# Performance work log

Measured on AMD Instinct MI355X. Metric: run time of the kernel, lower is better.

The kernel has to match this reference:

```python
import jax, jax.numpy as jnp
import numpy as np
import math

N_NODES = 50000
N_EDGES = 800000
IN_DIM = 128
HID = 128
OUT_DIM = 2048
N_LABEL_EDGES = 4096
POOL_RATIO = 0.5
NUM_HEADS = 8


def seg_sum(x, idx, n):
    return jax.ops.segment_sum(x, idx, num_segments=n)


def graph_conv(x, W, b, src, dst, emask, n):
    # DGL GraphConv, norm='both': D_out^-1/2 A D_in^-1/2 (x W) + b (masked edges)
    deg_out = seg_sum(emask, src, n)
    deg_in = seg_sum(emask, dst, n)
    ns = jax.lax.rsqrt(jnp.maximum(deg_out, 1.0))
    nd = jax.lax.rsqrt(jnp.maximum(deg_in, 1.0))
    h = x @ W
    msg = (h * ns[:, None])[src] * emask[:, None]
    agg = seg_sum(msg, dst, n)
    return agg * nd[:, None] + b


def conv_pool_block(x, src, dst, emask, cW, cb, sW, sb):
    # GraphConv -> ReLU -> SAGPool(top-k by GraphConv score, tanh gate) -> avg||max readout
    n = x.shape[0]
    h = jax.nn.relu(graph_conv(x, cW, cb, src, dst, emask, n))
    score = graph_conv(h, sW, sb, src, dst, emask, n)[:, 0]
    k = int(math.ceil(POOL_RATIO * n))  # static
    _, perm = jax.lax.top_k(score, k)
    h_new = h[perm] * jnp.tanh(score[perm])[:, None]
    # remap edges to the pooled node set; drop edges touching removed nodes via mask
    newid = jnp.full((n,), -1, jnp.int32).at[perm].set(jnp.arange(k, dtype=jnp.int32))
    nsrc = newid[src]
    ndst = newid[dst]
    new_mask = emask * (nsrc >= 0).astype(emask.dtype) * (ndst >= 0).astype(emask.dtype)
    nsrc = jnp.maximum(nsrc, 0)
    ndst = jnp.maximum(ndst, 0)
    readout = jnp.concatenate([h_new.mean(0), h_new.max(0)])[None, :]  # [1, 2*HID]
    return h_new, nsrc, ndst, new_mask, readout


def gat_conv(x, fcW, al, ar, lsrc, ldst, n, slope=0.2):
    # GATConv(1 -> 1, num_heads=8): head feature dim is 1
    h = x @ fcW                      # [n, heads]
    el = h * al
    er = h * ar
    e = jax.nn.leaky_relu(el[lsrc] + er[ldst], slope)  # [E_l, heads]
    emax = jax.ops.segment_max(e, ldst, num_segments=n)
    emax = jnp.where(jnp.isfinite(emax), emax, 0.0)
    ex = jnp.exp(e - emax[ldst])
    denom = seg_sum(ex, ldst, n)
    alpha = ex / jnp.maximum(denom[ldst], 1e-9)
    out = seg_sum(alpha * h[lsrc], ldst, n)            # [n, heads]
    return out[:, :, None]                             # [n, heads, 1]


def setup_inputs() -> dict:
    key = jax.random.key(0)
    ks = jax.random.split(key, 32)

    def rn(k, shape, s=0.05):
        return jax.random.normal(k, shape, jnp.float32) * s

    inp = {}
    inp['feat'] = jax.random.normal(ks[0], (N_NODES, IN_DIM), jnp.float32)
    inp['sequence_feature'] = jax.random.normal(ks[1], (1, 1024), jnp.float32)
    inp['src'] = jax.random.randint(ks[2], (N_EDGES,), 0, N_NODES, jnp.int32)
    inp['dst'] = jax.random.randint(ks[3], (N_EDGES,), 0, N_NODES, jnp.int32)
    inp['label_src'] = jax.random.randint(ks[4], (N_LABEL_EDGES,), 0, OUT_DIM, jnp.int32)
    inp['label_dst'] = jax.random.randint(ks[5], (N_LABEL_EDGES,), 0, OUT_DIM, jnp.int32)
    i = 6
    for b in range(3):
        din = IN_DIM if b == 0 else HID
        inp['cW%d' % b] = rn(ks[i], (din, HID)); i += 1
        inp['cb%d' % b] = jnp.zeros((HID,), jnp.float32)
        inp['sW%d' % b] = rn(ks[i], (HID, 1)); i += 1
        inp['sb%d' % b] = jnp.zeros((1,), jnp.float32)
    inp['lin1W'] = rn(ks[i], (2 * HID + 1024, 2 * HID)); i += 1
    inp['lin1b'] = jnp.zeros((2 * HID,), jnp.float32)
    inp['lin2W'] = rn(ks[i], (2 * HID, HID)); i += 1
    inp['lin2b'] = jnp.zeros((HID,), jnp.float32)
    inp['lin3W'] = rn(ks[i], (HID, OUT_DIM)); i += 1
    inp['lin3b'] = jnp.zeros((OUT_DIM,), jnp.float32)
    inp['gat_fcW'] = rn(ks[i], (1, NUM_HEADS)); i += 1
    inp['gat_al'] = rn(ks[i], (NUM_HEADS,)); i += 1
    inp['gat_ar'] = rn(ks[i], (NUM_HEADS,)); i += 1
    return inp


def reference(feat, sequence_feature, src, dst, label_src, label_dst,
              cW0, cb0, sW0, sb0, cW1, cb1, sW1, sb1, cW2, cb2, sW2, sb2,
              lin1W, lin1b, lin2W, lin2b, lin3W, lin3b,
              gat_fcW, gat_al, gat_ar):
    x, s, d = feat, src, dst
    emask = jnp.ones((src.shape[0],), jnp.float32)
    final = None
    for cW, cb, sW, sb in ((cW0, cb0, sW0, sb0), (cW1, cb1, sW1, sb1), (cW2, cb2, sW2, sb2)):
        x, s, d, emask, ro = conv_pool_block(x, s, d, emask, cW, cb, sW, sb)
        final = ro if final is None else final + ro
    final = jnp.concatenate([final, sequence_feature], axis=-1)  # [1, 2*HID+1024]
    f = jax.nn.relu(final @ lin1W + lin1b)
    # dropout: eval mode -> identity
    f = jax.nn.relu(f @ lin2W + lin2b)
    f = f @ lin3W + lin3b          # [1, OUT_DIM]
    ft = f.T                       # [OUT_DIM, 1]
    gat_out = gat_conv(ft, gat_fcW, gat_al, gat_ar, label_src, label_dst, OUT_DIM)
    max_value = jnp.max(gat_out, axis=1)      # [OUT_DIM, 1]
    _ = ft - jax.nn.relu(max_value)           # computed then discarded, as in source
    return ft.T
```

## Files before the change

kernel.cpp:

```cpp
#include <hip/hip_runtime.h>
#include <hip/hip_bf16.h>
#include <cmath>

#define N0 50000
#define NEDGE 800000
#define NEG_HUGE -3.402823466e38f
#define BMAX 64
#define STRIDE 128

typedef int i32x4 __attribute__((ext_vector_type(4)));
typedef __attribute__((ext_vector_type(8))) short short8v;
typedef __attribute__((ext_vector_type(4))) float f32x4;

__device__ inline float b2f(unsigned short u) { return __uint_as_float(((unsigned)u) << 16); }

__device__ inline unsigned short f2b(float f) {
    __hip_bfloat16 h = __float2bfloat16(f);
    return *(unsigned short*)&h;
}

__device__ inline unsigned fkey(float f) {
    unsigned b = __float_as_uint(f);
    if (b == 0x80000000u) b = 0u;
    return (b & 0x80000000u) ? ~b : (b | 0x80000000u);
}

__device__ inline void atomicMaxF(float* a, float v) {
    if (v >= 0.f) atomicMax((int*)a, __float_as_int(v));
    else          atomicMin((unsigned int*)a, __float_as_uint(v));
}

__global__ void k_init(float* finalv, float* f1raw, int* deg_out, int* fill,
                       int* binsA, int* binsB, float* maxbuf, int* ctrl) {
    int i = blockIdx.x * blockDim.x + threadIdx.x;
    if (i < 256) { finalv[i] = 0.f; f1raw[i] = 0.f; }
    if (i < 384) maxbuf[i] = NEG_HUGE;
    if (i < N0) { deg_out[i] = 0; fill[i] = 0; }
    if (i < 65536) { binsA[i] = 0; binsB[i] = 0; }
    if (i < 2) ctrl[8 + i] = 0;
}

__global__ __launch_bounds__(256) void k_remap(
        const int* __restrict__ esrc, const int* __restrict__ edst,
        const int2* __restrict__ ein, int use_pair,
        const int* __restrict__ ctrl, int slot,
        const int* __restrict__ newid,
        int2* __restrict__ eout, int* __restrict__ outcnt) {
    __shared__ int wbase[4];
    __shared__ int blkbase;
    int E = (slot < 0) ? NEDGE : ctrl[slot];
    if (blockIdx.x * 256 >= E) return;
    int i = blockIdx.x * 256 + threadIdx.x;
    int lane = threadIdx.x & 63, w = threadIdx.x >> 6;
    int ns = -1, nd = -1;
    if (i < E) {
        int s, d;
        if (use_pair) { int2 pr = ein[i]; s = pr.x; d = pr.y; }
        else { s = esrc[i]; d = edst[i]; }
        ns = newid[s]; nd = newid[d];
    }
    bool keep = (ns >= 0) && (nd >= 0);
    unsigned long long m = __ballot(keep);
    int rank = __popcll(m & ((1ull << lane) - 1ull));
    if (lane == 0) wbase[w] = __popcll(m);
    __syncthreads();
    if (threadIdx.x == 0)
        blkbase = atomicAdd(outcnt, wbase[0] + wbase[1] + wbase[2] + wbase[3]);
    __syncthreads();
    int base = blkbase;
    for (int q = 0; q < w; ++q) base += wbase[q];
    if (keep) eout[base + rank] = make_int2(ns, nd);
}

__global__ __launch_bounds__(256) void k_build(
        const int* __restrict__ esrc, const int* __restrict__ edst,
        const int2* __restrict__ epair, int use_pair,
        const int* __restrict__ ctrl, int slot, int n, int rsize,
        int* deg_out, int* fill, int* csr_src) {
    int E = (slot < 0) ? NEDGE : ctrl[slot];
    int r = blockIdx.x & 7;
    int lo = r * rsize;
    int hi = min(n, lo + rsize);
    int tpg = (int)(gridDim.x >> 3) * 256;
    int t = (int)(blockIdx.x >> 3) * 256 + threadIdx.x;
    for (int e0 = t * 8; e0 < E; e0 += tpg * 8) {
        int s[8], d[8];
        if (use_pair) {
            const i32x4* pp = (const i32x4*)(epair + e0);
#pragma unroll
            for (int q = 0; q < 4; ++q) {
                i32x4 a = __builtin_nontemporal_load(pp + q);
                s[q * 2] = a.x; d[q * 2] = a.y;
                s[q * 2 + 1] = a.z; d[q * 2 + 1] = a.w;
            }
        } else {
            const i32x4* ps = (const i32x4*)(esrc + e0);
            const i32x4* pd = (const i32x4*)(edst + e0);
#pragma unroll
            for (int q = 0; q < 2; ++q) {
                i32x4 a = __builtin_nontemporal_load(ps + q);
                i32x4 bq = __builtin_nontemporal_load(pd + q);
                s[q * 4] = a.x; s[q * 4 + 1] = a.y; s[q * 4 + 2] = a.z; s[q * 4 + 3] = a.w;
                d[q * 4] = bq.x; d[q * 4 + 1] = bq.y; d[q * 4 + 2] = bq.z; d[q * 4 + 3] = bq.w;
            }
        }
        int nrem = E - e0;
#pragma unroll
        for (int kq = 0; kq < 8; ++kq) {
            if (kq < nrem && d[kq] >= lo && d[kq] < hi) {
                atomicAdd(&deg_out[s[kq]], 1);
                int pos = atomicAdd(&fill[d[kq]], 1);
                if (pos < STRIDE) csr_src[(size_t)d[kq] * STRIDE + pos] = s[kq];
            }
        }
    }
}

__global__ __launch_bounds__(256) void k_gemm(
        const float* __restrict__ feat, const float* __restrict__ xprev,
        const int* __restrict__ oldid, const float* __restrict__ garr,
        const int* __restrict__ deg_out,
        const float* __restrict__ W, unsigned short* __restrict__ hpre,
        int n, int nprev, int mode) {
    __shared__ short Wt[128][136];
    __shared__ int ridx_s[64];
    __shared__ float esc_s[64];
    int tid = threadIdx.x;
    int r0 = blockIdx.x * 64;
    if (tid < 64) {
        int gr = r0 + tid;
        int ridx = 0; float esc = 0.f;
        if (gr < n) {
            if (mode == 0) {
                ridx = gr;
                esc = rsqrtf(fmaxf((float)deg_out[gr], 1.f));
            } else {
                int orow = oldid[gr];
                if ((unsigned)orow < (unsigned)nprev) {
                    ridx = orow;
                    esc = rsqrtf(fmaxf((float)deg_out[gr], 1.f)) * garr[gr];
                }
            }
        }
        ridx_s[tid] = ridx;
        esc_s[tid] = esc;
    }
    {
        int col = tid & 127;
        int kh = tid >> 7;
#pragma unroll
        for (int c8 = 0; c8 < 8; ++c8) {
            int kb = kh * 64 + c8 * 8;
            unsigned short v[8];
#pragma unroll
            for (int j = 0; j < 8; ++j)
                v[j] = f2b(W[(size_t)(kb + j) * 128 + col]);
            *(uint4*)&Wt[col][kb] = *(uint4*)v;
        }
    }
    __syncthreads();

    int lane = tid & 63, w = tid >> 6;
    const float* xsrc = (mode == 0) ? feat : xprev;
    int row16 = lane & 15;
    int ridx = ridx_s[w * 16 + row16];
    int ko = (lane >> 4) * 8;
    f32x4 acc[8];
#pragma unroll
    for (int t = 0; t < 8; ++t) acc[t] = (f32x4){0.f, 0.f, 0.f, 0.f};
#pragma unroll
    for (int kc = 0; kc < 4; ++kc) {
        int kbase = kc * 32 + ko;
        const float4* xp = (const float4*)(xsrc + (size_t)ridx * 128 + kbase);
        float4 fa = xp[0], fb = xp[1];
        unsigned short av[8];
        av[0] = f2b(fa.x); av[1] = f2b(fa.y); av[2] = f2b(fa.z); av[3] = f2b(fa.w);
        av[4] = f2b(fb.x); av[5] = f2b(fb.y); av[6] = f2b(fb.z); av[7] = f2b(fb.w);
        short8v a = *(short8v*)av;
#pragma unroll
        for (int t = 0; t < 8; ++t) {
            short8v b = *(short8v*)&Wt[t * 16 + row16][kbase];
            acc[t] = __builtin_amdgcn_mfma_f32_16x16x32_bf16(a, b, acc[t], 0, 0, 0);
        }
    }
    int rq = (lane >> 4) * 4;
    float esc[4];
#pragma unroll
    for (int r = 0; r < 4; ++r) esc[r] = esc_s[w * 16 + rq + r];
#pragma unroll
    for (int r = 0; r < 4; ++r) {
        int gr = r0 + w * 16 + rq + r;
        if (gr < n) {
            unsigned short* op = hpre + (size_t)gr * 128;
#pragma unroll
            for (int t = 0; t < 8; ++t)
                op[t * 16 + (lane & 15)] = f2b(acc[t][r] * esc[r]);
        }
    }
}

__global__ __launch_bounds__(256) void k_agg_conv(
        const unsigned short* __restrict__ hpre, const int* __restrict__ fill,
        const int* __restrict__ deg_out,
        const int* __restrict__ csr_src,
        const float* __restrict__ cb, const float* __restrict__ sW,
        float* __restrict__ hpost, float* __restrict__ hs, int n) {
    int wid = threadIdx.x >> 6;
    int lane = threadIdx.x & 63;
    int d = blockIdx.x * 4 + wid;
    if (d >= n) return;
    int degin = fill[d];
    int cnt = min(degin, STRIDE);
    const int* bp = csr_src + (size_t)d * STRIDE;
    float a0 = 0.f, a1 = 0.f;
    int j = 0;
    for (; j + 4 <= cnt; j += 4) {
        int4 ss = *(const int4*)(bp + j);
        ushort2 u0 = ((const ushort2*)(hpre + (size_t)ss.x * 128))[lane];
        ushort2 u1 = ((const ushort2*)(hpre + (size_t)ss.y * 128))[lane];
        ushort2 u2 = ((const ushort2*)(hpre + (size_t)ss.z * 128))[lane];
        ushort2 u3 = ((const ushort2*)(hpre + (size_t)ss.w * 128))[lane];
        a0 += (b2f(u0.x) + b2f(u1.x)) + (b2f(u2.x) + b2f(u3.x));
        a1 += (b2f(u0.y) + b2f(u1.y)) + (b2f(u2.y) + b2f(u3.y));
    }
    for (; j < cnt; ++j) {
        int s0 = bp[j];
        ushort2 u0 = ((const ushort2*)(hpre + (size_t)s0 * 128))[lane];
        a0 += b2f(u0.x);
        a1 += b2f(u0.y);
    }
    float nd2 = rsqrtf(fmaxf((float)degin, 1.f));
    int c0 = lane * 2;
    float h0 = fmaxf(fmaf(a0, nd2, cb[c0]), 0.f);
    float h1 = fmaxf(fmaf(a1, nd2, cb[c0 + 1]), 0.f);
    ((float2*)(hpost + (size_t)d * 128))[lane] = make_float2(h0, h1);
    float v = h0 * sW[c0] + h1 * sW[c0 + 1];
#pragma unroll
    for (int off = 32; off; off >>= 1) v += __shfl_down(v, off);
    if (lane == 0) hs[d] = v * rsqrtf(fmaxf((float)deg_out[d], 1.f));
}

__global__ void k_score_hist(const float* __restrict__ hs, const int* __restrict__ fill,
                             const int* __restrict__ csr_src,
                             const float* __restrict__ sb, float* score,
                             int* binsA, int n) {
    int d = blockIdx.x * blockDim.x + threadIdx.x;
    if (d >= n) return;
    int degin = fill[d];
    int cnt = min(degin, STRIDE);
    const int* bp = csr_src + (size_t)d * STRIDE;
    float sum = 0.f;
    int j = 0;
    for (; j + 4 <= cnt; j += 4) {
        int4 ss = *(const int4*)(bp + j);
        sum += (hs[ss.x] + hs[ss.y]) + (hs[ss.z] + hs[ss.w]);
    }
    for (; j < cnt; ++j) sum += hs[bp[j]];
    float sc = rsqrtf(fmaxf((float)degin, 1.f)) * sum + sb[0];
    score[d] = sc;
    atomicAdd(&binsA[fkey(sc) >> 16], 1);
}

__global__ void k_rhist2(const float* __restrict__ score, const int* __restrict__ ctrl,
                         int n, int* binsB) {
    unsigned p16 = (unsigned)ctrl[3];
    for (int i = blockIdx.x * 256 + threadIdx.x; i < n; i += gridDim.x * 256) {
        unsigned u = fkey(score[i]);
        if ((u >> 16) == p16) atomicAdd(&binsB[u & 0xFFFFu], 1);
    }
}

__global__ void k_rpick(int stage, int k0, int* ctrl, const int* __restrict__ bins) {
    __shared__ int gs[64];
    __shared__ int arr[1024];
    __shared__ int wsum[16];
    __shared__ int sChunk, sKrem;
    int t = threadIdx.x;
    {
        int c = t >> 4, sub = t & 15;
        const int4* p4 = (const int4*)(bins + (size_t)c * 1024);
        int s = 0;
#pragma unroll
        for (int q = 0; q < 16; ++q) {
            int4 v = p4[q * 16 + sub];
            s += v.x + v.y + v.z + v.w;
        }
#pragma unroll
        for (int off = 8; off; off >>= 1) s += __shfl_down(s, off, 16);
        if (sub == 0) gs[c] = s;
    }
    __syncthreads();
    if (t == 0) {
        int kneed = (stage == 0) ? k0 : ctrl[4];
        int cum = 0, c = 63;
        for (; c >= 1; --c) { int v = gs[c]; if (cum + v >= kneed) break; cum += v; }
        sChunk = c; sKrem = kneed - cum;
    }
    __syncthreads();
    int c = sChunk;
    int v = bins[(size_t)c * 1024 + t];
    arr[t] = v;
    int lane = t & 63, w = t >> 6;
    int s = v;
#pragma unroll
    for (int off = 32; off; off >>= 1) s += __shfl_down(s, off);
    if (lane == 0) wsum[w] = s;
    __syncthreads();
    if (t == 0) {
        int kneed = sKrem;
        int cum = 0, w2 = 15;
        for (; w2 >= 1; --w2) { int vv = wsum[w2]; if (cum + vv >= kneed) break; cum += vv; }
        int j = 63;
        for (; j >= 1; --j) { int vv = arr[w2 * 64 + j]; if (cum + vv >= kneed) break; cum += vv; }
        int bin = c * 1024 + w2 * 64 + j;
        if (stage == 0) { ctrl[3] = bin; ctrl[4] = kneed - cum; }
        else {
            ctrl[0] = (int)((((unsigned)ctrl[3]) << 16) | (unsigned)bin);
            ctrl[2] = kneed - cum;
        }
    }
}

__global__ void k_ccnt(const float* __restrict__ score, const int* __restrict__ ctrl,
                       int n, int* cntG, int* cntE) {
    __shared__ int wG[16], wE[16];
    int b = blockIdx.x;
    int i = b * 1024 + threadIdx.x;
    int lane = threadIdx.x & 63, wid = threadIdx.x >> 6;
    unsigned T = (unsigned)ctrl[0];
    bool inb = (i < n);
    unsigned u = inb ? fkey(score[i]) : 0u;
    bool isG = inb && (u > T);
    bool isE = inb && (u == T);
    unsigned long long mG = __ballot(isG);
    unsigned long long mE = __ballot(isE);
    if (lane == 0) { wG[wid] = __popcll(mG); wE[wid] = __popcll(mE); }
    __syncthreads();
    if (threadIdx.x == 0) {
        int sg = 0, se = 0;
#pragma unroll
        for (int w = 0; w < 16; ++w) { sg += wG[w]; se += wE[w]; }
        cntG[b] = sg; cntE[b] = se;
    }
}

__global__ void k_cemit(const float* __restrict__ score, const int* __restrict__ ctrl,
                        const int* __restrict__ cntG, const int* __restrict__ cntE,
                        int n, int knext, int* newid, int* oldid, float* garr,
                        int* deg_out, int* fill, int* binsA, int* binsB) {
    __shared__ int wG[16], wE[16];
    __shared__ int sGoff, sEoff;
    int b = blockIdx.x;
    int i = b * 1024 + threadIdx.x;
    if (knext > 0) {
        for (int z = i; z < 65536; z += gridDim.x * 1024) { binsA[z] = 0; binsB[z] = 0; }
        if (i < knext) { deg_out[i] = 0; fill[i] = 0; }
    }
    int lane = threadIdx.x & 63, wid = threadIdx.x >> 6;
    unsigned T = (unsigned)ctrl[0];
    int needEq = ctrl[2];
    bool inb = (i < n);
    float sc = inb ? score[i] : 0.f;
    unsigned u = inb ? fkey(sc) : 0u;
    bool isG = inb && (u > T);
    bool isE = inb && (u == T);
    unsigned long long mG = __ballot(isG);
    unsigned long long mE = __ballot(isE);
    if (lane == 0) { wG[wid] = __popcll(mG); wE[wid] = __popcll(mE); }
    if (threadIdx.x < 64) {
        int l = threadIdx.x;
        int vg = (l < b) ? cntG[l] : 0;
        int ve = (l < b) ? cntE[l] : 0;
#pragma unroll
        for (int off2 = 32; off2; off2 >>= 1) {
            vg += __shfl_down(vg, off2);
            ve += __shfl_down(ve, off2);
        }
        if (l == 0) { sGoff = vg; sEoff = ve; }
    }
    __syncthreads();
    unsigned long long below = (1ull << lane) - 1ull;
    int gW = 0, eW = 0;
    for (int w = 0; w < wid; ++w) { gW += wG[w]; eW += wE[w]; }
    int Gb = sGoff + gW + __popcll(mG & below);
    int Eb = sEoff + eW + __popcll(mE & below);
    if (inb) {
        bool sel = isG || (isE && (Eb < needEq));
        if (sel) {
            int j = Gb + min(Eb, needEq);
            newid[i] = j;
            oldid[j] = i;
            garr[j] = tanhf(sc);
        } else {
            newid[i] = -1;
        }
    }
}

__global__ void k_readout(const float* __restrict__ hpost, const int* __restrict__ oldid,
                          const float* __restrict__ garr, float* finalv, float* maxbuf,
                          int k, int n, float invk) {
    int c = threadIdx.x;
    float sum = 0.f, mx = NEG_HUGE;
    for (int r = blockIdx.x; r < k; r += gridDim.x) {
        int o = oldid[r];
        if ((unsigned)o >= (unsigned)n) continue;
        float g = garr[r];
        float v = hpost[(size_t)o * 128 + c] * g;
        sum += v;
        mx = fmaxf(mx, v);
    }
    atomicAdd(&finalv[c], sum * invk);
    atomicMaxF(&maxbuf[c], mx);
}

__global__ void k_mlp1(const float* __restrict__ finalv, const float* __restrict__ maxbuf,
                       const float* __restrict__ seq, const float* __restrict__ W1,
                       float* f1raw) {
    int o = threadIdx.x;
    int j0 = blockIdx.x * 128;
    float acc = 0.f;
    for (int jj = 0; jj < 128; ++jj) {
        int j = j0 + jj;
        float fv;
        if (j < 128) fv = finalv[j];
        else if (j < 256) fv = maxbuf[j - 128] + maxbuf[j] + maxbuf[j + 128];
        else fv = seq[j - 256];
        acc = fmaf(fv, W1[(size_t)j * 256 + o], acc);
    }
    atomicAdd(&f1raw[o], acc);
}

__global__ void k_mlp2(const float* __restrict__ f1raw, const float* __restrict__ b1,
                       const float* __restrict__ W2, const float* __restrict__ bb2,
                       float* f2v) {
    __shared__ float f1s[256];
    int t = threadIdx.x;
    f1s[t] = fmaxf(f1raw[t] + b1[t], 0.f);
    f1s[t + 128] = fmaxf(f1raw[t + 128] + b1[t + 128], 0.f);
    __syncthreads();
    float acc = 0.f;
    for (int j = 0; j < 256; ++j)
        acc = fmaf(f1s[j], W2[(size_t)j * 128 + t], acc);
    f2v[t] = fmaxf(acc + bb2[t], 0.f);
}

__global__ void k_mlp3(const float* __restrict__ f2v, const float* __restrict__ W3,
                       const float* __restrict__ b3, float* out) {
    __shared__ float f2s[128];
    int t = threadIdx.x;
    f2s[t] = f2v[t];
    __syncthreads();
    int col = blockIdx.x * 128 + t;
    float acc = 0.f;
    for (int j = 0; j < 128; ++j)
        acc = fmaf(f2s[j], W3[(size_t)j * 2048 + col], acc);
    out[col] = acc + b3[col];
}

extern "C" void kernel_launch(void* const* d_in, const int* in_sizes, int n_in,
                              void* d_out, int out_size, void* d_ws, size_t ws_size,
                              hipStream_t stream) {
    (void)in_sizes; (void)n_in; (void)out_size; (void)ws_size;
    const float* feat = (const float*)d_in[0];
    const float* seq  = (const float*)d_in[1];
    const int* src = (const int*)d_in[2];
    const int* dst = (const int*)d_in[3];
    const float *cW[3], *cb[3], *sW[3], *sb[3];
    for (int b = 0; b < 3; ++b) {
        cW[b] = (const float*)d_in[6 + 4 * b];
        cb[b] = (const float*)d_in[7 + 4 * b];
        sW[b] = (const float*)d_in[8 + 4 * b];
        sb[b] = (const float*)d_in[9 + 4 * b];
    }
    const float* lin1W = (const float*)d_in[18];
    const float* lin1b = (const float*)d_in[19];
    const float* lin2W = (const float*)d_in[20];
    const float* lin2b = (const float*)d_in[21];
    const float* lin3W = (const float*)d_in[22];
    const float* lin3b = (const float*)d_in[23];
    float* out = (float*)d_out;

    char* p = (char*)d_ws;
    size_t off = 0;
    auto alloc = [&](size_t bytes) -> void* {
        void* r = p + off;
        off = (off + bytes + 255) & ~(size_t)255;
        return r;
    };
    unsigned short* hpre = (unsigned short*)alloc((size_t)N0 * 128 * 2);
    float* hpost  = (float*)alloc((size_t)N0 * 128 * 4);
    float* hs     = (float*)alloc((size_t)N0 * 4);
    float* score  = (float*)alloc((size_t)N0 * 4);
    int* deg_out  = (int*)alloc((size_t)N0 * 4);
    int* fill     = (int*)alloc((size_t)N0 * 4);
    int2* epair1  = (int2*)alloc((size_t)NEDGE * 8);
    int* csr_src  = (int*)alloc((size_t)N0 * STRIDE * 4);
    int* newid    = (int*)alloc((size_t)N0 * 4);
    int* oldid    = (int*)alloc((size_t)25000 * 4);
    float* garr   = (float*)alloc((size_t)25000 * 4);
    float* maxbuf = (float*)alloc(3 * 128 * 4);
    float* finalv = (float*)alloc(256 * 4);
    float* f1raw  = (float*)alloc(256 * 4);
    float* f2v    = (float*)alloc(128 * 4);
    int* ctrl     = (int*)alloc(64 * 4);
    int* binsA    = (int*)alloc(65536 * 4);
    int* binsB    = (int*)alloc(65536 * 4);
    int* cntG     = (int*)alloc(BMAX * 4);
    int* cntE     = (int*)alloc(BMAX * 4);
    int2* epair2  = (int2*)hpre;

    const int nb[3] = {50000, 25000, 12500};
    const int kb[3] = {25000, 12500, 6250};
    const int rsz[3] = {6250, 3125, 1563};

    k_init<<<256, 256, 0, stream>>>(finalv, f1raw, deg_out, fill, binsA, binsB,
                                    maxbuf, ctrl);

    for (int b = 0; b < 3; ++b) {
        int n = nb[b], k = kb[b];
        int B = (n + 1023) / 1024;
        if (b == 1)
            k_remap<<<(NEDGE + 255) / 256, 256, 0, stream>>>(
                src, dst, (const int2*)0, 0, ctrl, -1, newid, epair1, ctrl + 8);
        else if (b == 2)
            k_remap<<<(NEDGE + 255) / 256, 256, 0, stream>>>(
                (const int*)0, (const int*)0, epair1, 1, ctrl, 8, newid, epair2, ctrl + 9);
        k_build<<<960, 256, 0, stream>>>(src, dst, (b == 1) ? epair1 : epair2,
                                         (b > 0) ? 1 : 0, ctrl,
                                         (b == 0) ? -1 : ((b == 1) ? 8 : 9),
                                         n, rsz[b], deg_out, fill, csr_src);
        k_gemm<<<(n + 63) / 64, 256, 0, stream>>>(feat, hpost, oldid, garr, deg_out, cW[b],
                                                  hpre, n, (b > 0) ? nb[b - 1] : 1,
                                                  (b == 0) ? 0 : 1);
        k_agg_conv<<<(n + 3) / 4, 256, 0, stream>>>(hpre, fill, deg_out, csr_src, cb[b],
                                                    sW[b], hpost, hs, n);
        k_score_hist<<<(n + 255) / 256, 256, 0, stream>>>(hs, fill, csr_src, sb[b],
                                                          score, binsA, n);
        k_rpick<<<1, 1024, 0, stream>>>(0, k, ctrl, binsA);
        k_rhist2<<<128, 256, 0, stream>>>(score, ctrl, n, binsB);
        k_rpick<<<1, 1024, 0, stream>>>(1, k, ctrl, binsB);
        k_ccnt<<<B, 1024, 0, stream>>>(score, ctrl, n, cntG, cntE);
        k_cemit<<<B, 1024, 0, stream>>>(score, ctrl, cntG, cntE, n, (b < 2) ? kb[b] : 0,
                                        newid, oldid, garr, deg_out, fill, binsA, binsB);
        k_readout<<<512, 128, 0, stream>>>(hpost, oldid, garr, finalv, maxbuf + b * 128,
                                           k, n, 1.0f / (float)k);
    }

    k_mlp1<<<10, 256, 0, stream>>>(finalv, maxbuf, seq, lin1W, f1raw);
    k_mlp2<<<1, 128, 0, stream>>>(f1raw, lin1b, lin2W, lin2b, f2v);
    k_mlp3<<<16, 128, 0, stream>>>(f2v, lin3W, lin3b, out);
}
```

Before: 618.9 us.

## Fuse edge remap with CSR build and stage GEMM input rows in LDS

Merges the edge-remap kernel into the CSR build so surviving edges update degree and CSR slots as they are compacted. This removes a separate build pass over the compacted edge list in blocks 1 and 2. The block-0 build drops the 8-way destination-range partitioning and uses one thread per 4 edges, so each edge is read once instead of by all 8 range groups. The GEMM now loads and converts its 64 input rows into a shared-memory tile cooperatively before the MFMA loop, in exchange for more LDS use and an extra barrier. Without the range partitioning, atomics on deg_out and fill land with less locality.

```diff
diff --git a/kernel.cpp b/kernel.cpp
--- a/kernel.cpp
+++ b/kernel.cpp
@@ -40,12 +40,31 @@
     if (i < 2) ctrl[8 + i] = 0;
 }
 
-__global__ __launch_bounds__(256) void k_remap(
+__global__ __launch_bounds__(256) void k_build(
+        const int* __restrict__ esrc, const int* __restrict__ edst,
+        int* deg_out, int* fill, int* csr_src) {
+    int t = blockIdx.x * 256 + threadIdx.x;
+    int e0 = t * 4;
+    if (e0 >= NEDGE) return;
+    i32x4 a = __builtin_nontemporal_load((const i32x4*)(esrc + e0));
+    i32x4 bq = __builtin_nontemporal_load((const i32x4*)(edst + e0));
+    int s[4] = {a.x, a.y, a.z, a.w};
+    int d[4] = {bq.x, bq.y, bq.z, bq.w};
+#pragma unroll
+    for (int kq = 0; kq < 4; ++kq) {
+        atomicAdd(&deg_out[s[kq]], 1);
+        int pos = atomicAdd(&fill[d[kq]], 1);
+        if (pos < STRIDE) csr_src[(size_t)d[kq] * STRIDE + pos] = s[kq];
+    }
+}
+
+__global__ __launch_bounds__(256) void k_rmbuild(
         const int* __restrict__ esrc, const int* __restrict__ edst,
         const int2* __restrict__ ein, int use_pair,
         const int* __restrict__ ctrl, int slot,
         const int* __restrict__ newid,
-        int2* __restrict__ eout, int* __restrict__ outcnt) {
+        int2* __restrict__ eout, int* __restrict__ outcnt,
+        int* deg_out, int* fill, int* csr_src) {
     __shared__ int wbase[4];
     __shared__ int blkbase;
     int E = (slot < 0) ? NEDGE : ctrl[slot];
@@ -69,50 +88,11 @@
     __syncthreads();
     int base = blkbase;
     for (int q = 0; q < w; ++q) base += wbase[q];
-    if (keep) eout[base + rank] = make_int2(ns, nd);
-}
-
-__global__ __launch_bounds__(256) void k_build(
-        const int* __restrict__ esrc, const int* __restrict__ edst,
-        const int2* __restrict__ epair, int use_pair,
-        const int* __restrict__ ctrl, int slot, int n, int rsize,
-        int* deg_out, int* fill, int* csr_src) {
-    int E = (slot < 0) ? NEDGE : ctrl[slot];
-    int r = blockIdx.x & 7;
-    int lo = r * rsize;
-    int hi = min(n, lo + rsize);
-    int tpg = (int)(gridDim.x >> 3) * 256;
-    int t = (int)(blockIdx.x >> 3) * 256 + threadIdx.x;
-    for (int e0 = t * 8; e0 < E; e0 += tpg * 8) {
-        int s[8], d[8];
-        if (use_pair) {
-            const i32x4* pp = (const i32x4*)(epair + e0);
-#pragma unroll
-            for (int q = 0; q < 4; ++q) {
-                i32x4 a = __builtin_nontemporal_load(pp + q);
-                s[q * 2] = a.x; d[q * 2] = a.y;
-                s[q * 2 + 1] = a.z; d[q * 2 + 1] = a.w;
-            }
-        } else {
-            const i32x4* ps = (const i32x4*)(esrc + e0);
-            const i32x4* pd = (const i32x4*)(edst + e0);
-#pragma unroll
-            for (int q = 0; q < 2; ++q) {
-                i32x4 a = __builtin_nontemporal_load(ps + q);
-                i32x4 bq = __builtin_nontemporal_load(pd + q);
-                s[q * 4] = a.x; s[q * 4 + 1] = a.y; s[q * 4 + 2] = a.z; s[q * 4 + 3] = a.w;
-                d[q * 4] = bq.x; d[q * 4 + 1] = bq.y; d[q * 4 + 2] = bq.z; d[q * 4 + 3] = bq.w;
-            }
-        }
-        int nrem = E - e0;
-#pragma unroll
-        for (int kq = 0; kq < 8; ++kq) {
-            if (kq < nrem && d[kq] >= lo && d[kq] < hi) {
-                atomicAdd(&deg_out[s[kq]], 1);
-                int pos = atomicAdd(&fill[d[kq]], 1);
-                if (pos < STRIDE) csr_src[(size_t)d[kq] * STRIDE + pos] = s[kq];
-            }
-        }
+    if (keep) {
+        eout[base + rank] = make_int2(ns, nd);
+        atomicAdd(&deg_out[ns], 1);
+        int pos = atomicAdd(&fill[nd], 1);
+        if (pos < STRIDE) csr_src[(size_t)nd * STRIDE + pos] = ns;
     }
 }
 
@@ -123,6 +103,7 @@
         const float* __restrict__ W, unsigned short* __restrict__ hpre,
         int n, int nprev, int mode) {
     __shared__ short Wt[128][136];
+    __shared__ short Xt[64][136];
     __shared__ int ridx_s[64];
     __shared__ float esc_s[64];
     int tid = threadIdx.x;
@@ -145,6 +126,7 @@
         ridx_s[tid] = ridx;
         esc_s[tid] = esc;
     }
+    __syncthreads();
     {
         int col = tid & 127;
         int kh = tid >> 7;
@@ -158,12 +140,23 @@
             *(uint4*)&Wt[col][kb] = *(uint4*)v;
         }
     }
+    {
+        const float* xsrc = (mode == 0) ? feat : xprev;
+        int rr = tid >> 2;
+        int kx = (tid & 3) * 32;
+        const float4* xp = (const float4*)(xsrc + (size_t)ridx_s[rr] * 128 + kx);
+#pragma unroll
+        for (int c4 = 0; c4 < 8; ++c4) {
+            float4 v = xp[c4];
+            unsigned short u[4];
+            u[0] = f2b(v.x); u[1] = f2b(v.y); u[2] = f2b(v.z); u[3] = f2b(v.w);
+            *(uint2*)&Xt[rr][kx + c4 * 4] = *(uint2*)u;
+        }
+    }
     __syncthreads();
 
     int lane = tid & 63, w = tid >> 6;
-    const float* xsrc = (mode == 0) ? feat : xprev;
     int row16 = lane & 15;
-    int ridx = ridx_s[w * 16 + row16];
     int ko = (lane >> 4) * 8;
     f32x4 acc[8];
 #pragma unroll
@@ -171,12 +164,7 @@
 #pragma unroll
     for (int kc = 0; kc < 4; ++kc) {
         int kbase = kc * 32 + ko;
-        const float4* xp = (const float4*)(xsrc + (size_t)ridx * 128 + kbase);
-        float4 fa = xp[0], fb = xp[1];
-        unsigned short av[8];
-        av[0] = f2b(fa.x); av[1] = f2b(fa.y); av[2] = f2b(fa.z); av[3] = f2b(fa.w);
-        av[4] = f2b(fb.x); av[5] = f2b(fb.y); av[6] = f2b(fb.z); av[7] = f2b(fb.w);
-        short8v a = *(short8v*)av;
+        short8v a = *(short8v*)&Xt[w * 16 + row16][kbase];
 #pragma unroll
         for (int t = 0; t < 8; ++t) {
             short8v b = *(short8v*)&Wt[t * 16 + row16][kbase];
@@ -512,7 +500,6 @@
 
     const int nb[3] = {50000, 25000, 12500};
     const int kb[3] = {25000, 12500, 6250};
-    const int rsz[3] = {6250, 3125, 1563};
 
     k_init<<<256, 256, 0, stream>>>(finalv, f1raw, deg_out, fill, binsA, binsB,
                                     maxbuf, ctrl);
@@ -520,16 +507,17 @@
     for (int b = 0; b < 3; ++b) {
         int n = nb[b], k = kb[b];
         int B = (n + 1023) / 1024;
-        if (b == 1)
-            k_remap<<<(NEDGE + 255) / 256, 256, 0, stream>>>(
-                src, dst, (const int2*)0, 0, ctrl, -1, newid, epair1, ctrl + 8);
-        else if (b == 2)
-            k_remap<<<(NEDGE + 255) / 256, 256, 0, stream>>>(
-                (const int*)0, (const int*)0, epair1, 1, ctrl, 8, newid, epair2, ctrl + 9);
-        k_build<<<960, 256, 0, stream>>>(src, dst, (b == 1) ? epair1 : epair2,
-                                         (b > 0) ? 1 : 0, ctrl,
-                                         (b == 0) ? -1 : ((b == 1) ? 8 : 9),
-                                         n, rsz[b], deg_out, fill, csr_src);
+        if (b == 0)
+            k_build<<<(NEDGE / 4 + 255) / 256, 256, 0, stream>>>(src, dst, deg_out, fill,
+                                                                 csr_src);
+        else if (b == 1)
+            k_rmbuild<<<(NEDGE + 255) / 256, 256, 0, stream>>>(
+                src, dst, (const int2*)0, 0, ctrl, -1, newid, epair1, ctrl + 8,
+                deg_out, fill, csr_src);
+        else
+            k_rmbuild<<<(NEDGE + 255) / 256, 256, 0, stream>>>(
+                (const int*)0, (const int*)0, epair1, 1, ctrl, 8, newid, epair2, ctrl + 9,
+                deg_out, fill, csr_src);
         k_gemm<<<(n + 63) / 64, 256, 0, stream>>>(feat, hpost, oldid, garr, deg_out, cW[b],
                                                   hpre, n, (b > 0) ? nb[b - 1] : 1,
                                                   (b == 0) ? 0 : 1);
```

Measured after the change: 594.4 us. 4.0% less time.
